# Kernel tuning notes

Measured on AMD Instinct MI355X. Metric: run time of the kernel, lower is better.

## Reference

```python
import jax, jax.numpy as jnp
import numpy as np

B, C, L = 8, 256, 1024
N_HEAD = 8
GROUPS = 32
EPS = 1e-5


def group_norm(x, gamma, beta):
    # x: [B, C, L]
    b, c, l = x.shape
    xg = x.reshape(b, GROUPS, (c // GROUPS) * l)
    mu = xg.mean(-1, keepdims=True)
    var = xg.var(-1, keepdims=True)
    xg = (xg - mu) / jnp.sqrt(var + EPS)
    x = xg.reshape(b, c, l)
    return x * gamma[None, :, None] + beta[None, :, None]


def conv1d(x, w, b=None, groups=1):
    # x: [B,C,L], w: [O, I/groups, K]
    k = w.shape[-1]
    pad = (k - 1) // 2
    y = jax.lax.conv_general_dilated(
        x, w, window_strides=(1,), padding=[(pad, pad)],
        dimension_numbers=('NCH', 'OIH', 'NCH'),
        feature_group_count=groups)
    if b is not None:
        y = y + b[None, :, None]
    return y


def setup_inputs() -> dict:
    key = jax.random.key(0)
    ks = jax.random.split(key, 8)
    x = jax.random.normal(ks[0], (B, C, L), dtype=jnp.float32)
    gamma = jnp.ones((C,), jnp.float32)
    beta = jnp.zeros((C,), jnp.float32)
    # depthwise conv: torch weight [C,1,3], kaiming_normal fan_in=1*3
    dw_w = jax.random.normal(ks[1], (C, 1, 3), jnp.float32) * np.sqrt(2.0 / 3.0)
    # qkv 1x1 conv: [3C, C, 1], kaiming fan_in=C
    qkv_w = jax.random.normal(ks[2], (3 * C, C, 1), jnp.float32) * np.sqrt(2.0 / C)
    qkv_b = jnp.zeros((3 * C,), jnp.float32)
    out_w = jax.random.normal(ks[3], (C, C, 1), jnp.float32) * np.sqrt(2.0 / C)
    out_b = jnp.zeros((C,), jnp.float32)
    return {"x": x, "gamma": gamma, "beta": beta, "dw_w": dw_w,
            "qkv_w": qkv_w, "qkv_b": qkv_b, "out_w": out_w, "out_b": out_b}


def reference(x, gamma, beta, dw_w, qkv_w, qkv_b, out_w, out_b):
    b, c, l = x.shape
    head_dim = c // N_HEAD
    h = group_norm(x, gamma, beta)
    h = conv1d(h, dw_w, groups=c)                 # depthwise k=3
    qkv = conv1d(h, qkv_w, qkv_b)                 # [B, 3C, L]
    qkv = qkv.reshape(b, N_HEAD, head_dim * 3, l)
    q, k, v = jnp.split(qkv, 3, axis=2)           # each [B, H, D, L]
    attn = jnp.einsum('bhdl,bhdL->bhlL', q, k) / jnp.sqrt(jnp.float32(c))
    attn = jax.nn.softmax(attn, axis=-1)
    o = jnp.einsum('bhlL,bhdL->bhdl', attn, v).reshape(b, c, l)
    o = conv1d(o, out_w, out_b)
    return o + x
```

## Files before the change

### kernel.cpp

```cpp
#include <hip/hip_runtime.h>
#include <hip/hip_bf16.h>

#define B_ 8
#define C_ 256
#define L_ 1024
#define NH_ 8
#define EPS_ 1e-5f

typedef __attribute__((ext_vector_type(8))) _Float16 half8;
typedef __attribute__((ext_vector_type(2))) __fp16 fp16x2;
typedef __attribute__((ext_vector_type(4))) float f32x4;

static __device__ inline ushort f2h(float f) {
  union { _Float16 h; ushort u; } c;
  c.h = (_Float16)f;
  return c.u;
}

static __device__ inline uint pkh(float a, float b) {
  union { fp16x2 v; uint u; } c;
  c.v = __builtin_amdgcn_cvt_pkrtz(a, b);
  return c.u;
}

__global__ __launch_bounds__(512) void gnw_kernel(
    const float* __restrict__ x, const float* __restrict__ gamma,
    const float* __restrict__ beta, const float* __restrict__ dw,
    const float4* __restrict__ qw, const float4* __restrict__ ow,
    uint2* __restrict__ wq, uint2* __restrict__ wo_,
    ushort* __restrict__ ht) {
  __shared__ float hn[8 * L_];
  __shared__ float ws0[8], ws1[8];
  int t = threadIdx.x;
  if (blockIdx.x < 128) {
    int id = blockIdx.x * 512 + t;
    float4 v;
    uint2* dst;
    if (id < 49152) { v = qw[id]; dst = wq + id; }
    else { v = ow[id - 49152]; dst = wo_ + (id - 49152); }
    *dst = make_uint2(pkh(v.x, v.y), pkh(v.z, v.w));
    return;
  }
  int blk = blockIdx.x - 128;
  int b = blk >> 5, g = blk & 31;
  const size_t base = ((size_t)(b * C_ + g * 8)) * L_;

  float s = 0.f, ss = 0.f;
  float vals[16];
#pragma unroll
  for (int i = 0; i < 16; ++i) {
    int e = t + 512 * i;
    float v = x[base + e];
    vals[i] = v;
    s += v; ss += v * v;
  }
#pragma unroll
  for (int off = 32; off >= 1; off >>= 1) {
    s  += __shfl_xor(s, off);
    ss += __shfl_xor(ss, off);
  }
  int wave = t >> 6;
  if ((t & 63) == 0) { ws0[wave] = s; ws1[wave] = ss; }
  __syncthreads();
  s = 0.f; ss = 0.f;
#pragma unroll
  for (int i = 0; i < 8; ++i) { s += ws0[i]; ss += ws1[i]; }
  float mean = s * (1.f / 8192.f);
  float var = ss * (1.f / 8192.f) - mean * mean;
  float rstd = rsqrtf(var + EPS_);

#pragma unroll
  for (int i = 0; i < 16; ++i) {
    int e = t + 512 * i;
    int c = g * 8 + (i >> 1);
    float sc = gamma[c] * rstd;
    hn[e] = (vals[i] - mean) * sc + beta[c];
  }
  __syncthreads();
  float r[16];
#pragma unroll
  for (int i = 0; i < 16; ++i) {
    int e = t + 512 * i;
    int l = e & 1023;
    int c = g * 8 + (i >> 1);
    float w0 = dw[c * 3 + 0], w1 = dw[c * 3 + 1], w2 = dw[c * 3 + 2];
    float a = (l > 0) ? hn[e - 1] : 0.f;
    float m = hn[e];
    float z = (l < 1023) ? hn[e + 1] : 0.f;
    r[i] = w0 * a + w1 * m + w2 * z;
  }
#pragma unroll
  for (int li = 0; li < 2; ++li) {
    int l = t + 512 * li;
    uint4 pk;
    pk.x = pkh(r[0 + li],  r[2 + li]);
    pk.y = pkh(r[4 + li],  r[6 + li]);
    pk.z = pkh(r[8 + li],  r[10 + li]);
    pk.w = pkh(r[12 + li], r[14 + li]);
    *(uint4*)(ht + (((size_t)(b * 32 + g)) * L_ + l) * 8) = pk;
  }
}

__global__ __launch_bounds__(256) void qkv_fused_kernel(
    const ushort* __restrict__ Xt, const ushort* __restrict__ Wb,
    const float* __restrict__ bias, ushort* __restrict__ qt,
    ushort* __restrict__ kt, ushort* __restrict__ vb) {
  int bx = blockIdx.x, head = blockIdx.y, b = blockIdx.z;
  int bh = b * 8 + head;
  int t = threadIdx.x;
  int w = t >> 6, l = t & 63;
  int g = l >> 4, ln = l & 15;
  int wl = w >> 1, wo = w & 1;
  int lbase = bx * 128 + wl * 64;

  const ushort* xb = Xt + (size_t)b * (32 * L_ * 8);
  const ushort* wp = Wb + (size_t)(head * 96 + wo * 48) * 256;

  f32x4 acc[4][3];
#pragma unroll
  for (int ml = 0; ml < 4; ++ml)
#pragma unroll
    for (int nn = 0; nn < 3; ++nn) acc[ml][nn] = (f32x4){0.f, 0.f, 0.f, 0.f};

  for (int c0 = 0; c0 < 256; c0 += 32) {
    half8 af[4], bf[3];
#pragma unroll
    for (int ml = 0; ml < 4; ++ml)
      af[ml] = *(const half8*)(xb +
          (((size_t)((c0 >> 3) + g)) * L_ + lbase + 16 * ml + ln) * 8);
#pragma unroll
    for (int nn = 0; nn < 3; ++nn)
      bf[nn] = *(const half8*)(wp + (size_t)(16 * nn + ln) * 256 + c0 + 8 * g);
#pragma unroll
    for (int ml = 0; ml < 4; ++ml)
#pragma unroll
      for (int nn = 0; nn < 3; ++nn)
        acc[ml][nn] = __builtin_amdgcn_mfma_f32_16x16x32_f16(af[ml], bf[nn], acc[ml][nn], 0, 0, 0);
  }

#pragma unroll
  for (int nn = 0; nn < 3; ++nn) {
    float bs = bias[head * 96 + wo * 48 + 16 * nn + ln];
#pragma unroll
    for (int ml = 0; ml < 4; ++ml)
#pragma unroll
      for (int r = 0; r < 4; ++r) acc[ml][nn][r] += bs;
  }

  __shared__ ushort tr[5120];
  const float QSC = 0.0625f * 1.44269504f;

  for (int rk = 0; rk < 2; ++rk) {
    float sc = rk ? 1.f : QSC;
    __syncthreads();
#pragma unroll
    for (int nn = 0; nn < 3; ++nn) {
      int ocl0 = wo * 48 + 16 * nn;
      if (ocl0 >= rk * 32 && ocl0 < rk * 32 + 32) {
        int d = ocl0 - rk * 32 + ln;
#pragma unroll
        for (int ml = 0; ml < 4; ++ml) {
          int lrow = wl * 64 + 16 * ml + 4 * g;
#pragma unroll
          for (int r = 0; r < 4; ++r)
            tr[(lrow + r) * 40 + d] = f2h(acc[ml][nn][r] * sc);
        }
      }
    }
    __syncthreads();
    {
      int row = t >> 1, half = t & 1;
      uint4 v0 = *(const uint4*)&tr[row * 40 + half * 16];
      uint4 v1 = *(const uint4*)&tr[row * 40 + half * 16 + 8];
      ushort* dst = (rk ? kt : qt) +
                    ((size_t)bh * L_ + bx * 128 + row) * 32 + half * 16;
      *(uint4*)dst = v0;
      *(uint4*)(dst + 8) = v1;
    }
  }

  __syncthreads();
  if (wo == 1) {
#pragma unroll
    for (int nn = 1; nn < 3; ++nn) {
      int d = 16 * (nn - 1) + ln;
#pragma unroll
      for (int ml = 0; ml < 4; ++ml) {
        int lc = wl * 64 + 16 * ml + 4 * g;
        *(uint2*)&tr[d * 136 + lc] =
            make_uint2(pkh(acc[ml][nn][0], acc[ml][nn][1]),
                       pkh(acc[ml][nn][2], acc[ml][nn][3]));
      }
    }
  }
  __syncthreads();
  {
    int d = t >> 3, s0 = t & 7;
    ushort* vdst = vb + ((size_t)bh * 32 + d) * L_ + bx * 128;
#pragma unroll
    for (int c = 0; c < 2; ++c) {
      int ch = s0 + 8 * c;
      int jj = ch >> 2, gg = ch & 3;
      uint2 lo = *(const uint2*)&tr[d * 136 + 32 * jj + 4 * gg];
      uint2 hi = *(const uint2*)&tr[d * 136 + 32 * jj + 16 + 4 * gg];
      *(uint4*)(vdst + 32 * jj + 8 * gg) = make_uint4(lo.x, lo.y, hi.x, hi.y);
    }
  }
}

__global__ __launch_bounds__(256) void outconv_kernel(
    const ushort* __restrict__ Xt, const ushort* __restrict__ Wb,
    const float* __restrict__ bias, const float* __restrict__ resid,
    float* __restrict__ out) {
  int b = blockIdx.z;
  int t = threadIdx.x;
  int w = t >> 6, l = t & 63;
  int g = l >> 4, ln = l & 15;
  int lbase = blockIdx.x * 128;
  int ocblk = blockIdx.y * 64;
  int ocbase = ocblk + w * 16;

  const ushort* xb = Xt + (size_t)b * (8 * L_ * 32);
  const ushort* wp = Wb + (size_t)ocbase * 256;

  f32x4 acc[8];
#pragma unroll
  for (int ml = 0; ml < 8; ++ml) acc[ml] = (f32x4){0.f, 0.f, 0.f, 0.f};

  for (int c0 = 0; c0 < 256; c0 += 32) {
    half8 af[8];
#pragma unroll
    for (int ml = 0; ml < 8; ++ml)
      af[ml] = *(const half8*)(xb +
          ((size_t)(c0 >> 5) * L_ + lbase + 16 * ml + ln) * 32 + 8 * g);
    half8 bf = *(const half8*)(wp + (size_t)ln * 256 + c0 + 8 * g);
#pragma unroll
    for (int ml = 0; ml < 8; ++ml)
      acc[ml] = __builtin_amdgcn_mfma_f32_16x16x32_f16(af[ml], bf, acc[ml], 0, 0, 0);
  }

  __shared__ float tile[64][132];
  float bs = bias[ocbase + ln];
#pragma unroll
  for (int ml = 0; ml < 8; ++ml) {
    int ll = 16 * ml + 4 * g;
    float4 v = make_float4(acc[ml][0] + bs, acc[ml][1] + bs,
                           acc[ml][2] + bs, acc[ml][3] + bs);
    *(float4*)&tile[w * 16 + ln][ll] = v;
  }
  __syncthreads();
  {
    int ocl = t >> 2, lq = t & 3;
    const float* src = &tile[ocl][lq * 32];
    size_t ob = ((size_t)b * 256 + ocblk + ocl) * L_ + lbase + lq * 32;
#pragma unroll
    for (int i = 0; i < 8; ++i) {
      float4 v = *(const float4*)(src + 4 * i);
      float4 rd = *(const float4*)(resid + ob + 4 * i);
      v.x += rd.x; v.y += rd.y; v.z += rd.z; v.w += rd.w;
      *(float4*)(out + ob + 4 * i) = v;
    }
  }
}

__global__ __launch_bounds__(256) void attn_mfma_kernel(
    const ushort* __restrict__ qt, const ushort* __restrict__ kt,
    const ushort* __restrict__ vb, ushort* __restrict__ ot) {
  const int id = blockIdx.x;
  const int bh = ((id & 7) << 3) | (id >> 6);
  const int qtile = (id >> 3) & 7;
  const int t = threadIdx.x;
  const int w = t >> 6, l = t & 63;
  const int g = l >> 4, ln = l & 15;
  const int q0b = qtile * 128;
  const int q0 = q0b + w * 32;

  __shared__ __align__(16) ushort smem[18944];

  const ushort* qbase = qt + (size_t)bh * (L_ * 32);
  const ushort* kbase = kt + (size_t)bh * (L_ * 32);
  const ushort* vbase = vb + (size_t)bh * (32 * L_);

  const int krow = t >> 1, khalf = t & 1;
  const ushort* kg = kbase + krow * 32 + khalf * 16;
  const int kwo = krow * 40 + khalf * 16;
  const int vrow = t >> 3, vc = (t & 7) * 16;
  const ushort* vg = vbase + (size_t)vrow * L_ + vc;
  const int vwo = vrow * 136 + vc;

  const f32x4 z4 = {0.f, 0.f, 0.f, 0.f};
  half8 bq[2];
  bq[0] = *(const half8*)(qbase + (size_t)(q0 + ln) * 32 + g * 8);
  bq[1] = *(const half8*)(qbase + (size_t)(q0 + 16 + ln) * 32 + g * 8);

  union { ushort s[8]; half8 v; } onesu;
#pragma unroll
  for (int i = 0; i < 8; ++i) onesu.s[i] = 0x3C00;
  const half8 ones = onesu.v;

  f32x4 oacc[2][2];
  oacc[0][0] = z4; oacc[0][1] = z4; oacc[1][0] = z4; oacc[1][1] = z4;
  f32x4 oaccS[2] = {z4, z4};

  uint4 ka0, ka1, va0, va1;
  ka0 = *(const uint4*)kg;       ka1 = *(const uint4*)(kg + 8);
  va0 = *(const uint4*)vg;       va1 = *(const uint4*)(vg + 8);
  __builtin_amdgcn_sched_barrier(0);
  *(uint4*)&smem[kwo] = ka0;             *(uint4*)&smem[kwo + 8] = ka1;
  *(uint4*)&smem[10240 + vwo] = va0;     *(uint4*)&smem[10240 + vwo + 8] = va1;
  asm volatile("s_waitcnt lgkmcnt(0)" ::: "memory");
  __builtin_amdgcn_s_barrier();
  __builtin_amdgcn_sched_barrier(0);

  for (int tt = 0; tt < 8; ++tt) {
    const int cur = tt & 1;
    if (tt < 7) {
      ka0 = *(const uint4*)(kg + (tt + 1) * 4096);
      ka1 = *(const uint4*)(kg + (tt + 1) * 4096 + 8);
      va0 = *(const uint4*)(vg + (tt + 1) * 128);
      va1 = *(const uint4*)(vg + (tt + 1) * 128 + 8);
    }
    __builtin_amdgcn_sched_barrier(0);

    const ushort* Kc = &smem[cur * 5120];
    const ushort* Vc = &smem[10240 + cur * 4352];

    f32x4 sacc[8][2];
#pragma unroll
    for (int mk = 0; mk < 8; ++mk) {
      half8 ak = *(const half8*)(Kc + (16 * mk + ln) * 40 + g * 8);
      sacc[mk][0] = __builtin_amdgcn_mfma_f32_16x16x32_f16(ak, bq[0], z4, 0, 0, 0);
      sacc[mk][1] = __builtin_amdgcn_mfma_f32_16x16x32_f16(ak, bq[1], z4, 0, 0, 0);
    }

    uint upk[2][8][2];
#pragma unroll
    for (int nq = 0; nq < 2; ++nq) {
#pragma unroll
      for (int mk = 0; mk < 8; ++mk) {
        float e0 = __builtin_amdgcn_exp2f(sacc[mk][nq][0]);
        float e1 = __builtin_amdgcn_exp2f(sacc[mk][nq][1]);
        float e2 = __builtin_amdgcn_exp2f(sacc[mk][nq][2]);
        float e3 = __builtin_amdgcn_exp2f(sacc[mk][nq][3]);
        upk[nq][mk][0] = pkh(e0, e1);
        upk[nq][mk][1] = pkh(e2, e3);
      }
    }

#pragma unroll
    for (int ks = 0; ks < 4; ++ks) {
      union { uint u[4]; half8 v; } pb0, pb1;
      pb0.u[0] = upk[0][2 * ks][0]; pb0.u[1] = upk[0][2 * ks][1];
      pb0.u[2] = upk[0][2 * ks + 1][0]; pb0.u[3] = upk[0][2 * ks + 1][1];
      pb1.u[0] = upk[1][2 * ks][0]; pb1.u[1] = upk[1][2 * ks][1];
      pb1.u[2] = upk[1][2 * ks + 1][0]; pb1.u[3] = upk[1][2 * ks + 1][1];
      oaccS[0] = __builtin_amdgcn_mfma_f32_16x16x32_f16(ones, pb0.v, oaccS[0], 0, 0, 0);
      oaccS[1] = __builtin_amdgcn_mfma_f32_16x16x32_f16(ones, pb1.v, oaccS[1], 0, 0, 0);
#pragma unroll
      for (int md = 0; md < 2; ++md) {
        half8 av = *(const half8*)(Vc + (16 * md + ln) * 136 + 32 * ks + 8 * g);
        oacc[md][0] = __builtin_amdgcn_mfma_f32_16x16x32_f16(av, pb0.v, oacc[md][0], 0, 0, 0);
        oacc[md][1] = __builtin_amdgcn_mfma_f32_16x16x32_f16(av, pb1.v, oacc[md][1], 0, 0, 0);
      }
    }

    __builtin_amdgcn_sched_barrier(0);
    if (tt < 7) {
      const int nxt = cur ^ 1;
      *(uint4*)&smem[nxt * 5120 + kwo] = ka0;
      *(uint4*)&smem[nxt * 5120 + kwo + 8] = ka1;
      *(uint4*)&smem[10240 + nxt * 4352 + vwo] = va0;
      *(uint4*)&smem[10240 + nxt * 4352 + vwo + 8] = va1;
      asm volatile("s_waitcnt lgkmcnt(0)" ::: "memory");
      __builtin_amdgcn_s_barrier();
      __builtin_amdgcn_sched_barrier(0);
    }
  }

  ushort* otile = &smem[0];
  float rl0 = 1.f / oaccS[0][0];
  float rl1 = 1.f / oaccS[1][0];
#pragma unroll
  for (int md = 0; md < 2; ++md) {
    uint2 p0 = make_uint2(pkh(oacc[md][0][0] * rl0, oacc[md][0][1] * rl0),
                          pkh(oacc[md][0][2] * rl0, oacc[md][0][3] * rl0));
    uint2 p1 = make_uint2(pkh(oacc[md][1][0] * rl1, oacc[md][1][1] * rl1),
                          pkh(oacc[md][1][2] * rl1, oacc[md][1][3] * rl1));
    *(uint2*)&otile[(w * 32 + ln) * 40 + 16 * md + 4 * g] = p0;
    *(uint2*)&otile[(w * 32 + 16 + ln) * 40 + 16 * md + 4 * g] = p1;
  }
  __syncthreads();
  {
    int row = t >> 1, half = t & 1;
    uint4 v0 = *(const uint4*)&otile[row * 40 + half * 16];
    uint4 v1 = *(const uint4*)&otile[row * 40 + half * 16 + 8];
    ushort* dstp = ot + ((size_t)bh * L_ + q0b + row) * 32 + half * 16;
    *(uint4*)dstp = v0;
    *(uint4*)(dstp + 8) = v1;
  }
}

extern "C" void kernel_launch(void* const* d_in, const int* in_sizes, int n_in,
                              void* d_out, int out_size, void* d_ws, size_t ws_size,
                              hipStream_t stream) {
  const float* x      = (const float*)d_in[0];
  const float* gamma  = (const float*)d_in[1];
  const float* beta   = (const float*)d_in[2];
  const float* dw     = (const float*)d_in[3];
  const float* qkv_w  = (const float*)d_in[4];
  const float* qkv_b  = (const float*)d_in[5];
  const float* out_w  = (const float*)d_in[6];
  const float* out_b  = (const float*)d_in[7];
  float* out = (float*)d_out;

  char* ws = (char*)d_ws;
  ushort* ht   = (ushort*)(ws);
  ushort* qtb  = (ushort*)(ws + (16u << 20));
  ushort* ktb  = (ushort*)(ws + (20u << 20));
  ushort* vbb  = (ushort*)(ws + (24u << 20));
  ushort* otb  = (ushort*)(ws);
  ushort* wq   = (ushort*)(ws + (28u << 20));
  ushort* wo   = (ushort*)(ws + (28u << 20) + (512u << 10));

  gnw_kernel<<<384, 512, 0, stream>>>(x, gamma, beta, dw,
                                      (const float4*)qkv_w, (const float4*)out_w,
                                      (uint2*)wq, (uint2*)wo, ht);
  qkv_fused_kernel<<<dim3(8, 8, B_), 256, 0, stream>>>(ht, wq, qkv_b, qtb, ktb, vbb);
  attn_mfma_kernel<<<512, 256, 0, stream>>>(qtb, ktb, vbb, otb);
  outconv_kernel<<<dim3(8, 4, B_), 256, 0, stream>>>(otb, wo, out_b, x, out);
}
```

Measured before the change: 54.25 us.

## Split attention KV range across two wave groups and merge partial results

```diff
diff --git a/kernel.cpp b/kernel.cpp
--- a/kernel.cpp
+++ b/kernel.cpp
@@ -263,7 +263,7 @@
   }
 }
 
-__global__ __launch_bounds__(256) void attn_mfma_kernel(
+__global__ __launch_bounds__(512) void attn_mfma_kernel(
     const ushort* __restrict__ qt, const ushort* __restrict__ kt,
     const ushort* __restrict__ vb, ushort* __restrict__ ot) {
   const int id = blockIdx.x;
@@ -272,21 +272,22 @@
   const int t = threadIdx.x;
   const int w = t >> 6, l = t & 63;
   const int g = l >> 4, ln = l & 15;
+  const int quad = w >> 2, wq = w & 3;
   const int q0b = qtile * 128;
-  const int q0 = q0b + w * 32;
-
-  __shared__ __align__(16) ushort smem[18944];
+  const int q0 = q0b + wq * 32;
+  const int kvbase = quad * 512;
+
+  __shared__ __align__(16) ushort smem[20480];
 
   const ushort* qbase = qt + (size_t)bh * (L_ * 32);
   const ushort* kbase = kt + (size_t)bh * (L_ * 32);
   const ushort* vbase = vb + (size_t)bh * (32 * L_);
 
-  const int krow = t >> 1, khalf = t & 1;
-  const ushort* kg = kbase + krow * 32 + khalf * 16;
+  const int tq = t & 255;
+  const int krow = tq >> 1, khalf = tq & 1;
+  const ushort* kg = kbase + (size_t)(kvbase + krow) * 32 + khalf * 16;
+  const int kldsbase = quad * 10240;
   const int kwo = krow * 40 + khalf * 16;
-  const int vrow = t >> 3, vc = (t & 7) * 16;
-  const ushort* vg = vbase + (size_t)vrow * L_ + vc;
-  const int vwo = vrow * 136 + vc;
 
   const f32x4 z4 = {0.f, 0.f, 0.f, 0.f};
   half8 bq[2];
@@ -302,28 +303,24 @@
   oacc[0][0] = z4; oacc[0][1] = z4; oacc[1][0] = z4; oacc[1][1] = z4;
   f32x4 oaccS[2] = {z4, z4};
 
-  uint4 ka0, ka1, va0, va1;
+  uint4 ka0, ka1;
   ka0 = *(const uint4*)kg;       ka1 = *(const uint4*)(kg + 8);
-  va0 = *(const uint4*)vg;       va1 = *(const uint4*)(vg + 8);
   __builtin_amdgcn_sched_barrier(0);
-  *(uint4*)&smem[kwo] = ka0;             *(uint4*)&smem[kwo + 8] = ka1;
-  *(uint4*)&smem[10240 + vwo] = va0;     *(uint4*)&smem[10240 + vwo + 8] = va1;
+  *(uint4*)&smem[kldsbase + kwo] = ka0;
+  *(uint4*)&smem[kldsbase + kwo + 8] = ka1;
   asm volatile("s_waitcnt lgkmcnt(0)" ::: "memory");
   __builtin_amdgcn_s_barrier();
   __builtin_amdgcn_sched_barrier(0);
 
-  for (int tt = 0; tt < 8; ++tt) {
+  for (int tt = 0; tt < 4; ++tt) {
     const int cur = tt & 1;
-    if (tt < 7) {
+    if (tt < 3) {
       ka0 = *(const uint4*)(kg + (tt + 1) * 4096);
       ka1 = *(const uint4*)(kg + (tt + 1) * 4096 + 8);
-      va0 = *(const uint4*)(vg + (tt + 1) * 128);
-      va1 = *(const uint4*)(vg + (tt + 1) * 128 + 8);
     }
     __builtin_amdgcn_sched_barrier(0);
 
-    const ushort* Kc = &smem[cur * 5120];
-    const ushort* Vc = &smem[10240 + cur * 4352];
+    const ushort* Kc = &smem[kldsbase + cur * 5120];
 
     f32x4 sacc[8][2];
 #pragma unroll
@@ -347,6 +344,8 @@
       }
     }
 
+    const ushort* vt = vbase + kvbase + tt * 128;
+    __builtin_amdgcn_s_setprio(1);
 #pragma unroll
     for (int ks = 0; ks < 4; ++ks) {
       union { uint u[4]; half8 v; } pb0, pb1;
@@ -358,42 +357,61 @@
       oaccS[1] = __builtin_amdgcn_mfma_f32_16x16x32_f16(ones, pb1.v, oaccS[1], 0, 0, 0);
 #pragma unroll
       for (int md = 0; md < 2; ++md) {
-        half8 av = *(const half8*)(Vc + (16 * md + ln) * 136 + 32 * ks + 8 * g);
+        half8 av = *(const half8*)(vt + (size_t)(16 * md + ln) * L_ + 32 * ks + 8 * g);
         oacc[md][0] = __builtin_amdgcn_mfma_f32_16x16x32_f16(av, pb0.v, oacc[md][0], 0, 0, 0);
         oacc[md][1] = __builtin_amdgcn_mfma_f32_16x16x32_f16(av, pb1.v, oacc[md][1], 0, 0, 0);
       }
     }
+    __builtin_amdgcn_s_setprio(0);
 
     __builtin_amdgcn_sched_barrier(0);
-    if (tt < 7) {
+    if (tt < 3) {
       const int nxt = cur ^ 1;
-      *(uint4*)&smem[nxt * 5120 + kwo] = ka0;
-      *(uint4*)&smem[nxt * 5120 + kwo + 8] = ka1;
-      *(uint4*)&smem[10240 + nxt * 4352 + vwo] = va0;
-      *(uint4*)&smem[10240 + nxt * 4352 + vwo + 8] = va1;
+      *(uint4*)&smem[kldsbase + nxt * 5120 + kwo] = ka0;
+      *(uint4*)&smem[kldsbase + nxt * 5120 + kwo + 8] = ka1;
       asm volatile("s_waitcnt lgkmcnt(0)" ::: "memory");
       __builtin_amdgcn_s_barrier();
       __builtin_amdgcn_sched_barrier(0);
     }
   }
 
-  ushort* otile = &smem[0];
-  float rl0 = 1.f / oaccS[0][0];
-  float rl1 = 1.f / oaccS[1][0];
-#pragma unroll
-  for (int md = 0; md < 2; ++md) {
-    uint2 p0 = make_uint2(pkh(oacc[md][0][0] * rl0, oacc[md][0][1] * rl0),
-                          pkh(oacc[md][0][2] * rl0, oacc[md][0][3] * rl0));
-    uint2 p1 = make_uint2(pkh(oacc[md][1][0] * rl1, oacc[md][1][1] * rl1),
-                          pkh(oacc[md][1][2] * rl1, oacc[md][1][3] * rl1));
-    *(uint2*)&otile[(w * 32 + ln) * 40 + 16 * md + 4 * g] = p0;
-    *(uint2*)&otile[(w * 32 + 16 + ln) * 40 + 16 * md + 4 * g] = p1;
-  }
-  __syncthreads();
-  {
+  float* Of = (float*)&smem[10240];
+  float* Df = (float*)&smem[18688];
+  if (quad == 1) {
+#pragma unroll
+    for (int nq = 0; nq < 2; ++nq) {
+      int qrow = wq * 32 + nq * 16 + ln;
+#pragma unroll
+      for (int md = 0; md < 2; ++md) {
+        *(float4*)&Of[qrow * 33 + 16 * md + 4 * g] =
+            make_float4(oacc[md][nq][0], oacc[md][nq][1],
+                        oacc[md][nq][2], oacc[md][nq][3]);
+      }
+      Df[qrow] = oaccS[nq][0];
+    }
+  }
+  __syncthreads();
+  if (quad == 0) {
+    ushort* otile = &smem[0];
+#pragma unroll
+    for (int nq = 0; nq < 2; ++nq) {
+      int qrow = wq * 32 + nq * 16 + ln;
+      float rl = 1.f / (oaccS[nq][0] + Df[qrow]);
+#pragma unroll
+      for (int md = 0; md < 2; ++md) {
+        float4 p = *(const float4*)&Of[qrow * 33 + 16 * md + 4 * g];
+        uint2 pk = make_uint2(
+            pkh((oacc[md][nq][0] + p.x) * rl, (oacc[md][nq][1] + p.y) * rl),
+            pkh((oacc[md][nq][2] + p.z) * rl, (oacc[md][nq][3] + p.w) * rl));
+        *(uint2*)&otile[qrow * 40 + 16 * md + 4 * g] = pk;
+      }
+    }
+  }
+  __syncthreads();
+  if (t < 256) {
     int row = t >> 1, half = t & 1;
-    uint4 v0 = *(const uint4*)&otile[row * 40 + half * 16];
-    uint4 v1 = *(const uint4*)&otile[row * 40 + half * 16 + 8];
+    uint4 v0 = *(const uint4*)&smem[row * 40 + half * 16];
+    uint4 v1 = *(const uint4*)&smem[row * 40 + half * 16 + 8];
     ushort* dstp = ot + ((size_t)bh * L_ + q0b + row) * 32 + half * 16;
     *(uint4*)dstp = v0;
     *(uint4*)(dstp + 8) = v1;
@@ -426,6 +444,6 @@
                                       (const float4*)qkv_w, (const float4*)out_w,
                                       (uint2*)wq, (uint2*)wo, ht);
   qkv_fused_kernel<<<dim3(8, 8, B_), 256, 0, stream>>>(ht, wq, qkv_b, qtb, ktb, vbb);
-  attn_mfma_kernel<<<512, 256, 0, stream>>>(qtb, ktb, vbb, otb);
+  attn_mfma_kernel<<<512, 512, 0, stream>>>(qtb, ktb, vbb, otb);
   outconv_kernel<<<dim3(8, 4, B_), 256, 0, stream>>>(otb, wo, out_b, x, out);
 }
```

Result: slower. 59.21 us (+9.1%).
